# Kernel tuning notes

Measured on AMD Instinct MI355X. Metric: run time of the kernel, lower is better.

## Reference

```python
import jax, jax.numpy as jnp
import numpy as np

B, L, H, NH, DH, FF, NL, REL = 2, 1024, 256, 8, 32, 1024, 2, 100
SCALE = np.sqrt(DH).astype(np.float32)
EPS = 1e-5


def _ln(x, g, b):
    m = jnp.mean(x, axis=-1, keepdims=True)
    v = jnp.mean(jnp.square(x - m), axis=-1, keepdims=True)
    return (x - m) * jax.lax.rsqrt(v + EPS) * g + b


def setup_inputs() -> dict:
    key = jax.random.key(0)
    ks = jax.random.split(key, 20)
    s = 0.02
    Ek = jax.random.normal(ks[0], (REL, DH), jnp.float32) * s
    Ev = jax.random.normal(ks[1], (REL, DH), jnp.float32) * s
    Ek = Ek.at[0].set(0.0)  # padding_idx=0
    Ev = Ev.at[0].set(0.0)
    return {
        "inputs": jax.random.normal(ks[2], (B, L, H), jnp.float32),
        "Wq": jax.random.normal(ks[3], (NL, H, H), jnp.float32) * s,
        "Wk": jax.random.normal(ks[4], (NL, H, H), jnp.float32) * s,
        "Wv": jax.random.normal(ks[5], (NL, H, H), jnp.float32) * s,
        "Wo": jax.random.normal(ks[6], (NL, H, H), jnp.float32) * s,
        "bo": jnp.zeros((NL, H), jnp.float32),
        "W1": jax.random.normal(ks[7], (NL, H, FF), jnp.float32) * s,
        "b1": jnp.zeros((NL, FF), jnp.float32),
        "W2": jax.random.normal(ks[8], (NL, FF, H), jnp.float32) * s,
        "b2": jnp.zeros((NL, H), jnp.float32),
        "ln1_g": jnp.ones((NL, H), jnp.float32),
        "ln1_b": jnp.zeros((NL, H), jnp.float32),
        "ln2_g": jnp.ones((NL, H), jnp.float32),
        "ln2_b": jnp.zeros((NL, H), jnp.float32),
        "Ek": Ek,
        "Ev": Ev,
        "relations": jax.random.randint(ks[9], (B, L, L), 0, REL, jnp.int32),
        "relations_mask": jax.random.randint(ks[10], (B, L, L), 0, 2, jnp.int32).astype(bool),
    }


def reference(inputs, Wq, Wk, Wv, Wo, bo, W1, b1, W2, b2,
              ln1_g, ln1_b, ln2_g, ln2_b, Ek, Ev, relations, relations_mask):
    # relation embeddings shared across layers and heads: (B,L,L,DH)
    rel_k = Ek[relations]
    rel_v = Ev[relations]
    neg = relations_mask.astype(jnp.float32) * (-1e20)  # (B,L,L)
    x = inputs
    for l in range(NL):
        q = (x @ Wq[l]).reshape(B, L, NH, DH)
        k = (x @ Wk[l]).reshape(B, L, NH, DH)
        v = (x @ Wv[l]).reshape(B, L, NH, DH)
        # scores: q.(k_j + rel_k[i,j]) decomposed to avoid (B,H,L,L,DH)
        e = (jnp.einsum('bihd,bjhd->bhij', q, k)
             + jnp.einsum('bihd,bijd->bhij', q, rel_k)) / SCALE
        e = e + neg[:, None, :, :]
        a = jax.nn.softmax(e, axis=-1)  # (B,NH,L,L)
        o = (jnp.einsum('bhij,bjhd->bihd', a, v)
             + jnp.einsum('bhij,bijd->bihd', a, rel_v)).reshape(B, L, H)
        o = o @ Wo[l] + bo[l]
        x = _ln(x + o, ln1_g[l], ln1_b[l])
        ff = jax.nn.relu(x @ W1[l] + b1[l]) @ W2[l] + b2[l]
        x = _ln(x + ff, ln2_g[l], ln2_b[l])
    return x
```

## Files before the change

### kernel.cpp

```cpp
#include <hip/hip_runtime.h>


typedef unsigned short ushortt;
typedef __attribute__((ext_vector_type(8))) short short8;
typedef __attribute__((ext_vector_type(4))) float f32x4;

__device__ __forceinline__ ushortt f2bf(float f) {
  union { float f; unsigned int u; } c; c.f = f;
  unsigned int r = c.u + 0x7fffu + ((c.u >> 16) & 1u);
  return (ushortt)(r >> 16);
}
__device__ __forceinline__ unsigned int pk2(float a, float b) {
  return (unsigned int)f2bf(a) | ((unsigned int)f2bf(b) << 16);
}

__global__ void wcvt_all_k(const float* __restrict__ Wq, const float* __restrict__ Wk,
                           const float* __restrict__ Wv, const float* __restrict__ Wo,
                           const float* __restrict__ W1, const float* __restrict__ W2,
                           ushortt* __restrict__ wbuf) {
  int i = blockIdx.x * blockDim.x + threadIdx.x;
  int st = gridDim.x * blockDim.x;
  for (; i < 1572864; i += st) {
    int l = (i >= 786432) ? 1 : 0;
    int e = i - (l ? 786432 : 0);
    size_t o_w = (size_t)l * 65536, o_w1 = (size_t)l * 262144;
    float v;
    if (e < 262144) {
      int which = e >> 16;
      int loc = e & 65535;
      int k = loc & 255, n = loc >> 8;
      const float* W = (which == 0) ? Wq : (which == 1) ? Wk : (which == 2) ? Wv : Wo;
      v = W[o_w + ((size_t)k << 8) + n];
    } else if (e < 524288) {
      int loc = e - 262144;
      int k = loc & 255, n = loc >> 8;
      v = W1[o_w1 + ((size_t)k << 10) + n];
    } else {
      int loc = e - 524288;
      int k = loc & 1023, n = loc >> 10;
      v = W2[o_w1 + ((size_t)k << 8) + n];
    }
    wbuf[i] = f2bf(v);
  }
}

__global__ __launch_bounds__(256) void cvt_bf_k(
    const float* __restrict__ in, ushortt* __restrict__ out, int n) {
  int idx = (blockIdx.x * 256 + threadIdx.x) * 8;
  if (idx >= n) return;
  float4 f0 = *(const float4*)(in + idx);
  float4 f1 = *(const float4*)(in + idx + 4);
  uint4 u;
  u.x = pk2(f0.x, f0.y); u.y = pk2(f0.z, f0.w);
  u.z = pk2(f1.x, f1.y); u.w = pk2(f1.z, f1.w);
  *(uint4*)(out + idx) = u;
}

__global__ __launch_bounds__(256) void relpack_k(
    const int* __restrict__ rel, const int* __restrict__ msk,
    unsigned char* __restrict__ relc2,
    const float* __restrict__ Ev, float* __restrict__ EvT) {
  int g = blockIdx.x * blockDim.x + threadIdx.x;
  const int4* r4 = (const int4*)rel;
  const int4* m4 = (const int4*)msk;
  int4 r = r4[g];
  int4 m = m4[g];
  int b = g >> 18;
  int rem = g & 262143;
  int i = rem >> 8;
  int j4 = (rem & 255) << 2;
  size_t base = ((size_t)b << 20) + ((size_t)(i >> 3) << 13) + (i & 7);
  relc2[base + ((size_t)(j4 + 0) << 3)] = (unsigned char)(m.x ? 128 : r.x);
  relc2[base + ((size_t)(j4 + 1) << 3)] = (unsigned char)(m.y ? 128 : r.y);
  relc2[base + ((size_t)(j4 + 2) << 3)] = (unsigned char)(m.z ? 128 : r.z);
  relc2[base + ((size_t)(j4 + 3) << 3)] = (unsigned char)(m.w ? 128 : r.w);
  if (g < 3200) {
    int d = g / 100, rr = g - d * 100;
    EvT[d * 100 + rr] = Ev[(rr << 5) + d];
  }
}

__device__ __forceinline__ void mgemm_body(
    const ushortt* __restrict__ A, const ushortt* __restrict__ BT,
    const float* __restrict__ bias, size_t boff,
    float* __restrict__ C, ushortt* __restrict__ cbf,
    int m0, int n0, int N, int K, int kbeg, int kend, int relu, int kvmode)
{
  __shared__ ushortt As[64 * 72];
  __shared__ ushortt Bs[64 * 72];
  int tid = threadIdx.x;
  int wv = tid >> 6, lane = tid & 63;
  int quad = lane >> 4, mr = lane & 15;
  int sm = tid >> 2, k16 = (tid & 3) << 4;

  const ushortt* ap = A + (size_t)(m0 + sm) * K + k16;
  const ushortt* bp = BT + (size_t)(n0 + sm) * K + k16;

  uint4 ra0 = *(const uint4*)(ap + kbeg);
  uint4 ra1 = *(const uint4*)(ap + kbeg + 8);
  uint4 rb0 = *(const uint4*)(bp + kbeg);
  uint4 rb1 = *(const uint4*)(bp + kbeg + 8);

  f32x4 acc[4] = {};
  for (int k0 = kbeg; k0 < kend; k0 += 64) {
    *(uint4*)(&As[sm * 72 + k16])     = ra0;
    *(uint4*)(&As[sm * 72 + k16 + 8]) = ra1;
    *(uint4*)(&Bs[sm * 72 + k16])     = rb0;
    *(uint4*)(&Bs[sm * 72 + k16 + 8]) = rb1;
    __syncthreads();
    if (k0 + 64 < kend) {
      ra0 = *(const uint4*)(ap + k0 + 64);
      ra1 = *(const uint4*)(ap + k0 + 72);
      rb0 = *(const uint4*)(bp + k0 + 64);
      rb1 = *(const uint4*)(bp + k0 + 72);
    }
#pragma unroll
    for (int kh = 0; kh < 2; ++kh) {
      short8 af = *(const short8*)(&As[(wv * 16 + mr) * 72 + (kh << 5) + quad * 8]);
#pragma unroll
      for (int nt = 0; nt < 4; ++nt) {
        short8 bf = *(const short8*)(&Bs[(nt * 16 + mr) * 72 + (kh << 5) + quad * 8]);
        acc[nt] = __builtin_amdgcn_mfma_f32_16x16x32_bf16(af, bf, acc[nt], 0, 0, 0);
      }
    }
    __syncthreads();
  }
#pragma unroll
  for (int nt = 0; nt < 4; ++nt) {
#pragma unroll
    for (int r = 0; r < 4; ++r) {
      int m = m0 + wv * 16 + quad * 4 + r;
      int n = n0 + nt * 16 + mr;
      float v = acc[nt][r];
      if (bias) v += bias[boff + n];
      if (relu) v = fmaxf(v, 0.f);
      if (kvmode == 1) {
        int b = m >> 10, i = m & 1023, h = n >> 5, d = n & 31;
        cbf[(size_t)(((b << 3) + h) * 32 + d) * 1024 + i] = f2bf(v);
      } else if (kvmode == 2) {
        int b = m >> 10, i = m & 1023, h = n >> 5, d = n & 31;
        cbf[(size_t)(((b << 3) + h) * 1024 + i) * 32 + d] = f2bf(v);
      } else if (cbf) {
        cbf[(size_t)m * N + n] = f2bf(v);
      } else {
        C[(size_t)m * N + n] = v;
      }
    }
  }
}

__global__ __launch_bounds__(256) void mgemm_k(
    const ushortt* __restrict__ A, const ushortt* __restrict__ BT,
    const float* __restrict__ bias, size_t boff,
    float* __restrict__ C0, float* __restrict__ C1, ushortt* __restrict__ cbf,
    int N, int K, int relu)
{
  int kidx = blockIdx.z;
  int kc = K / gridDim.z;
  int kbeg = kidx * kc;
  mgemm_body(A, BT, kidx ? nullptr : bias, boff,
             kidx ? C1 : C0, cbf,
             blockIdx.y * 64, blockIdx.x * 64, N, K, kbeg, kbeg + kc, relu, 0);
}

__global__ __launch_bounds__(256) void mqkv_k(
    const ushortt* __restrict__ xbf, const ushortt* __restrict__ WT,
    float* __restrict__ q, ushortt* __restrict__ kbf, ushortt* __restrict__ vTbf)
{
  int sel = blockIdx.x >> 2;
  const ushortt* BT = WT + (size_t)sel * 65536;
  int mode = (sel == 1) ? 2 : (sel == 2) ? 1 : 0;
  mgemm_body(xbf, BT, nullptr, 0,
             (sel == 0) ? q : nullptr,
             (sel == 1) ? kbf : (sel == 2) ? vTbf : nullptr,
             blockIdx.y * 64, (blockIdx.x & 3) * 64, 256, 256, 0, 256, 0, mode);
}

__global__ __launch_bounds__(256) void attn_mf8_k(
    const float* __restrict__ q, const ushortt* __restrict__ kbf,
    const ushortt* __restrict__ vTbf, const float* __restrict__ Ek,
    const float* __restrict__ EvT, const unsigned char* __restrict__ relc2,
    ushortt* __restrict__ out)
{
  __shared__ ushortt pbf[8 * 1028];
  __shared__ float regA[1072];
  __shared__ float wbin[8 * 108];

  int tid = threadIdx.x;
  int wv = tid >> 6, lane = tid & 63;
  int quad = lane >> 4, mr = lane & 15;
  int tile = blockIdx.x & 127;
  int h = (blockIdx.x >> 7) & 7;
  int b = blockIdx.x >> 10;
  int i0 = tile << 3;

  int iqsel = quad & 1;
  int iq = iqsel << 2;
  int jofs = ((quad >> 1) << 4) + mr;
  int jbase = wv << 8;
  const unsigned int* rc2 =
      (const unsigned int*)(relc2 + (((size_t)(b << 7) + tile) << 13));
  unsigned int rcw[8];
#pragma unroll
  for (int t = 0; t < 8; ++t)
    rcw[t] = rc2[(((jbase + (t << 5) + jofs)) << 1) + iqsel];

  float* qs = regA;
  float* expq = regA + 264;

  {
    int i = tid >> 5, d = tid & 31;
    qs[i * 33 + d] = q[(((size_t)(b * 1024 + i0 + i) * 8 + h) << 5) + d]
                     * 0.17677669529663687f;
  }
  for (int p = tid; p < 864; p += 256) wbin[p] = 0.f;
  __syncthreads();

  for (int p = tid; p < 800; p += 256) {
    int i = p / 100, r = p - i * 100;
    const float* ep = Ek + (r << 5);
    float s = 0.f;
#pragma unroll
    for (int d = 0; d < 32; ++d) s += qs[i * 33 + d] * ep[d];
    expq[i * 101 + r] = __expf(s);
  }
  __syncthreads();

  short8 qf;
#pragma unroll
  for (int jj = 0; jj < 8; ++jj)
    ((ushortt*)&qf)[jj] = f2bf(qs[(mr & 7) * 33 + quad * 8 + jj]);

  const ushortt* ks = kbf + ((size_t)(b * 8 + h) << 15);
  const ushortt* vs = vTbf + ((size_t)(b * 8 + h) << 15);

  short8 kfa = *(const short8*)(ks + ((size_t)(jbase + mr) << 5) + quad * 8);
  short8 kfb = *(const short8*)(ks + ((size_t)(jbase + 16 + mr) << 5) + quad * 8);
#pragma unroll
  for (int t = 0; t < 8; ++t) {
    int j0 = jbase + (t << 5);
    short8 ka = kfa, kb = kfb;
    if (t < 7) {
      kfa = *(const short8*)(ks + ((size_t)(j0 + 32 + mr) << 5) + quad * 8);
      kfb = *(const short8*)(ks + ((size_t)(j0 + 48 + mr) << 5) + quad * 8);
    }
    f32x4 z = {};
    f32x4 sa = __builtin_amdgcn_mfma_f32_16x16x32_bf16(qf, ka, z, 0, 0, 0);
    f32x4 sb = __builtin_amdgcn_mfma_f32_16x16x32_bf16(qf, kb, z, 0, 0, 0);
    int j = j0 + jofs;
    unsigned int w = rcw[t];
#pragma unroll
    for (int r = 0; r < 4; ++r) {
      int i = iq + r;
      float sv = (quad >= 2) ? sb[r] : sa[r];
      unsigned int c = (w >> (r << 3)) & 255u;
      float p = 0.f;
      if (c < 128u) {
        p = __expf(sv) * expq[i * 101 + (int)c];
        atomicAdd(&wbin[i * 108 + (int)c], p);
      }
      pbf[i * 1028 + j] = f2bf(p);
    }
  }
  __syncthreads();

  float* pvpart = regA;
  float* pvtot  = regA + 256;
  int d0 = (wv & 1) << 4;
  int k0 = (wv >> 1) << 9;
  int prow = (mr & 7) * 1028;
  f32x4 acc0 = {}, acc1 = {};
  short8 vf = *(const short8*)(vs + ((size_t)(d0 + mr) << 10) + k0 + quad * 8);
#pragma unroll
  for (int kt = 0; kt < 16; ++kt) {
    int kk = k0 + (kt << 5);
    short8 vcur = vf;
    if (kt < 15)
      vf = *(const short8*)(vs + ((size_t)(d0 + mr) << 10) + k0 + ((kt + 1) << 5) + quad * 8);
    short8 pf = *(const short8*)(&pbf[prow + kk + quad * 8]);
    if (kt & 1)
      acc1 = __builtin_amdgcn_mfma_f32_16x16x32_bf16(pf, vcur, acc1, 0, 0, 0);
    else
      acc0 = __builtin_amdgcn_mfma_f32_16x16x32_bf16(pf, vcur, acc0, 0, 0, 0);
  }
  f32x4 acc;
#pragma unroll
  for (int r = 0; r < 4; ++r) acc[r] = acc0[r] + acc1[r];
  if (wv >= 2 && quad < 2) {
#pragma unroll
    for (int r = 0; r < 4; ++r)
      pvpart[((wv & 1) << 7) + (quad * 4 + r) * 16 + mr] = acc[r];
  }
  __syncthreads();
  if (wv < 2 && quad < 2) {
#pragma unroll
    for (int r = 0; r < 4; ++r) {
      int i = quad * 4 + r;
      pvtot[i * 32 + d0 + mr] = acc[r] + pvpart[((wv & 1) << 7) + i * 16 + mr];
    }
  }
  __syncthreads();

  {
    int i = tid >> 5, d = tid & 31;
    const float4* evt = (const float4*)(EvT + d * 100);
    const float4* wb4 = (const float4*)(&wbin[i * 108]);
    float e0 = 0.f, e1 = 0.f, e2 = 0.f, e3 = 0.f;
    float s0 = 0.f, s1 = 0.f, s2 = 0.f, s3 = 0.f;
#pragma unroll
    for (int rq = 0; rq < 25; ++rq) {
      float4 e4 = evt[rq];
      float4 w4 = wb4[rq];
      e0 += w4.x * e4.x; s0 += w4.x;
      e1 += w4.y * e4.y; s1 += w4.y;
      e2 += w4.z * e4.z; s2 += w4.z;
      e3 += w4.w * e4.w; s3 += w4.w;
    }
    float ev = (e0 + e1) + (e2 + e3);
    float den = (s0 + s1) + (s2 + s3);
    out[(((size_t)(b * 1024 + i0 + i) * 8 + h) << 5) + d] =
        f2bf((pvtot[i * 32 + d] + ev) / den);
  }
}

__global__ __launch_bounds__(256) void ln_k(
    const float* __restrict__ x, const float* __restrict__ o,
    const float* __restrict__ o2,
    const float* __restrict__ g, const float* __restrict__ bta, size_t eoff,
    float* __restrict__ xo, ushortt* __restrict__ xbf, float* __restrict__ fout)
{
  __shared__ float red[256];
  int row = blockIdx.x, t = threadIdx.x;
  size_t idx = (size_t)row * 256 + t;
  float r = x[idx] + o[idx];
  if (o2) r += o2[idx];
  red[t] = r;
  __syncthreads();
  for (int off = 128; off > 0; off >>= 1) {
    if (t < off) red[t] += red[t + off];
    __syncthreads();
  }
  float mean = red[0] * (1.f / 256.f);
  __syncthreads();
  float dv = r - mean;
  red[t] = dv * dv;
  __syncthreads();
  for (int off = 128; off > 0; off >>= 1) {
    if (t < off) red[t] += red[t + off];
    __syncthreads();
  }
  float var = red[0] * (1.f / 256.f);
  float val = dv * rsqrtf(var + 1e-5f) * g[eoff + t] + bta[eoff + t];
  xo[idx] = val;
  xbf[idx] = f2bf(val);
  if (fout) fout[idx] = val;
}

extern "C" void kernel_launch(void* const* d_in, const int* in_sizes, int n_in,
                              void* d_out, int out_size, void* d_ws, size_t ws_size,
                              hipStream_t stream) {
  const float* inp  = (const float*)d_in[0];
  const float* Wq   = (const float*)d_in[1];
  const float* Wk   = (const float*)d_in[2];
  const float* Wv   = (const float*)d_in[3];
  const float* Wo   = (const float*)d_in[4];
  const float* bo   = (const float*)d_in[5];
  const float* W1   = (const float*)d_in[6];
  const float* b1   = (const float*)d_in[7];
  const float* W2   = (const float*)d_in[8];
  const float* b2   = (const float*)d_in[9];
  const float* ln1g = (const float*)d_in[10];
  const float* ln1b = (const float*)d_in[11];
  const float* ln2g = (const float*)d_in[12];
  const float* ln2b = (const float*)d_in[13];
  const float* Ek   = (const float*)d_in[14];
  const float* Ev   = (const float*)d_in[15];
  const int*   rel  = (const int*)d_in[16];
  const int*   msk  = (const int*)d_in[17];

  const size_t SZ = 524288;
  float* x        = (float*)d_ws;
  float* q        = x + SZ;
  ushortt* kbf    = (ushortt*)(q + SZ);
  ushortt* vTbf   = kbf + SZ;
  ushortt* attnbf = vTbf + SZ;
  ushortt* xbf    = attnbf + SZ;
  float* tmp      = (float*)(xbf + SZ);
  ushortt* wbuf   = (ushortt*)(tmp + SZ);
  unsigned char* relc2 = (unsigned char*)(wbuf + 1572864);
  float* EvT      = (float*)(relc2 + 2097152);
  float* tmp2     = (float*)((char*)EvT + 16384);
  ushortt* inpbf  = (ushortt*)tmp2;
  ushortt* ffh    = (ushortt*)q;

  dim3 blk(256);
  wcvt_all_k<<<3072, blk, 0, stream>>>(Wq, Wk, Wv, Wo, W1, W2, wbuf);
  relpack_k<<<2048, blk, 0, stream>>>(rel, msk, relc2, Ev, EvT);
  cvt_bf_k<<<256, blk, 0, stream>>>(inp, inpbf, 524288);

  for (int l = 0; l < 2; ++l) {
    size_t o_b  = (size_t)l * 256;
    size_t o_b1 = (size_t)l * 1024;
    const ushortt* xinbf = (l == 0) ? inpbf : xbf;
    const float* xin = (l == 0) ? inp : x;
    ushortt* wl = wbuf + (size_t)l * 786432;

    mqkv_k<<<dim3(12, 32), blk, 0, stream>>>(xinbf, wl, q, kbf, vTbf);

    attn_mf8_k<<<2048, blk, 0, stream>>>(q, kbf, vTbf, Ek, EvT, relc2, attnbf);

    mgemm_k<<<dim3(4, 32, 2), blk, 0, stream>>>(attnbf, wl + 196608,
                                                bo, o_b, tmp, tmp2, nullptr,
                                                256, 256, 0);
    ln_k<<<2048, blk, 0, stream>>>(xin, tmp, tmp2, ln1g, ln1b, o_b, x, xbf, nullptr);

    mgemm_k<<<dim3(16, 32, 1), blk, 0, stream>>>(xbf, wl + 262144,
                                                 b1, o_b1, nullptr, nullptr, ffh,
                                                 1024, 256, 1);
    mgemm_k<<<dim3(4, 32, 2), blk, 0, stream>>>(ffh, wl + 524288,
                                                b2, o_b, tmp, tmp2, nullptr,
                                                256, 1024, 0);
    ln_k<<<2048, blk, 0, stream>>>(x, tmp, tmp2, ln2g, ln2b, o_b, x, xbf,
                                   (l == 1) ? (float*)d_out : nullptr);
  }
}
```

Before: 387.5 us.

## Split q·Ek exponent table into separate kernel and emit pre-scaled bf16 q

Moves the per-tile exp(q·Ek) relation-score table out of the attention kernel into a new eqk_k kernel that stages Ek in shared memory and writes the table to global memory. The QKV GEMM now also writes a pre-scaled bf16 copy of q in head-major layout, so attention loads its MFMA fragment directly instead of converting from fp32 shared memory. This removes one barrier and the serial dot-product prologue from the attention kernel, aiming to shorten its critical path and shrink its shared memory. The cost is an extra launch and a global round trip of about 6.5 MB for the table per layer.

Measured after the change: 372.1 us. -4.0%, faster.

```diff
diff --git a/kernel.cpp b/kernel.cpp
--- a/kernel.cpp
+++ b/kernel.cpp
@@ -80,6 +80,37 @@
   }
 }
 
+__global__ __launch_bounds__(256) void eqk_k(
+    const float* __restrict__ q, const float* __restrict__ Ek,
+    float* __restrict__ eqk) {
+  __shared__ float qs[8 * 33];
+  __shared__ float ek[100 * 33];
+  int tid = threadIdx.x;
+  int bid = blockIdx.x;
+  int tile = bid & 127;
+  int h = (bid >> 7) & 7;
+  int b = bid >> 10;
+  int i0 = tile << 3;
+  {
+    int i = tid >> 5, d = tid & 31;
+    qs[i * 33 + d] = q[(((size_t)(b * 1024 + i0 + i) * 8 + h) << 5) + d]
+                     * 0.17677669529663687f;
+  }
+  for (int p = tid; p < 3200; p += 256) {
+    int r = p >> 5, d = p & 31;
+    ek[r * 33 + d] = Ek[p];
+  }
+  __syncthreads();
+  float* eo = eqk + (size_t)bid * 800;
+  for (int p = tid; p < 800; p += 256) {
+    int i = p / 100, r = p - i * 100;
+    float s = 0.f;
+#pragma unroll
+    for (int d = 0; d < 32; ++d) s += qs[i * 33 + d] * ek[r * 33 + d];
+    eo[p] = __expf(s);
+  }
+}
+
 __device__ __forceinline__ void mgemm_body(
     const ushortt* __restrict__ A, const ushortt* __restrict__ BT,
     const float* __restrict__ bias, size_t boff,
@@ -134,7 +165,12 @@
       float v = acc[nt][r];
       if (bias) v += bias[boff + n];
       if (relu) v = fmaxf(v, 0.f);
-      if (kvmode == 1) {
+      if (kvmode == 3) {
+        C[(size_t)m * N + n] = v;
+        int b = m >> 10, i = m & 1023, h = n >> 5, d = n & 31;
+        cbf[(size_t)(((b << 3) + h) * 1024 + i) * 32 + d] =
+            f2bf(v * 0.17677669529663687f);
+      } else if (kvmode == 1) {
         int b = m >> 10, i = m & 1023, h = n >> 5, d = n & 31;
         cbf[(size_t)(((b << 3) + h) * 32 + d) * 1024 + i] = f2bf(v);
       } else if (kvmode == 2) {
@@ -165,33 +201,35 @@
 
 __global__ __launch_bounds__(256) void mqkv_k(
     const ushortt* __restrict__ xbf, const ushortt* __restrict__ WT,
-    float* __restrict__ q, ushortt* __restrict__ kbf, ushortt* __restrict__ vTbf)
+    float* __restrict__ q, ushortt* __restrict__ qbf,
+    ushortt* __restrict__ kbf, ushortt* __restrict__ vTbf)
 {
   int sel = blockIdx.x >> 2;
   const ushortt* BT = WT + (size_t)sel * 65536;
-  int mode = (sel == 1) ? 2 : (sel == 2) ? 1 : 0;
+  int mode = (sel == 0) ? 3 : (sel == 1) ? 2 : 1;
   mgemm_body(xbf, BT, nullptr, 0,
              (sel == 0) ? q : nullptr,
-             (sel == 1) ? kbf : (sel == 2) ? vTbf : nullptr,
+             (sel == 0) ? qbf : (sel == 1) ? kbf : vTbf,
              blockIdx.y * 64, (blockIdx.x & 3) * 64, 256, 256, 0, 256, 0, mode);
 }
 
 __global__ __launch_bounds__(256) void attn_mf8_k(
-    const float* __restrict__ q, const ushortt* __restrict__ kbf,
-    const ushortt* __restrict__ vTbf, const float* __restrict__ Ek,
+    const ushortt* __restrict__ qbf, const ushortt* __restrict__ kbf,
+    const ushortt* __restrict__ vTbf, const float* __restrict__ eqk,
     const float* __restrict__ EvT, const unsigned char* __restrict__ relc2,
     ushortt* __restrict__ out)
 {
   __shared__ ushortt pbf[8 * 1028];
-  __shared__ float regA[1072];
+  __shared__ float expq[800];
   __shared__ float wbin[8 * 108];
 
   int tid = threadIdx.x;
   int wv = tid >> 6, lane = tid & 63;
   int quad = lane >> 4, mr = lane & 15;
-  int tile = blockIdx.x & 127;
-  int h = (blockIdx.x >> 7) & 7;
-  int b = blockIdx.x >> 10;
+  int bid = blockIdx.x;
+  int tile = bid & 127;
+  int h = (bid >> 7) & 7;
+  int b = bid >> 10;
   int i0 = tile << 3;
 
   int iqsel = quad & 1;
@@ -205,37 +243,19 @@
   for (int t = 0; t < 8; ++t)
     rcw[t] = rc2[(((jbase + (t << 5) + jofs)) << 1) + iqsel];
 
-  float* qs = regA;
-  float* expq = regA + 264;
-
-  {
-    int i = tid >> 5, d = tid & 31;
-    qs[i * 33 + d] = q[(((size_t)(b * 1024 + i0 + i) * 8 + h) << 5) + d]
-                     * 0.17677669529663687f;
-  }
+  const float* eo = eqk + (size_t)bid * 800;
+  for (int p = tid; p < 800; p += 256) expq[p] = eo[p];
   for (int p = tid; p < 864; p += 256) wbin[p] = 0.f;
-  __syncthreads();
-
-  for (int p = tid; p < 800; p += 256) {
-    int i = p / 100, r = p - i * 100;
-    const float* ep = Ek + (r << 5);
-    float s = 0.f;
-#pragma unroll
-    for (int d = 0; d < 32; ++d) s += qs[i * 33 + d] * ep[d];
-    expq[i * 101 + r] = __expf(s);
-  }
-  __syncthreads();
-
-  short8 qf;
-#pragma unroll
-  for (int jj = 0; jj < 8; ++jj)
-    ((ushortt*)&qf)[jj] = f2bf(qs[(mr & 7) * 33 + quad * 8 + jj]);
+
+  const ushortt* qsrc = qbf + ((size_t)(b * 8 + h) << 15);
+  short8 qf = *(const short8*)(qsrc + (((size_t)i0 + (mr & 7)) << 5) + quad * 8);
 
   const ushortt* ks = kbf + ((size_t)(b * 8 + h) << 15);
   const ushortt* vs = vTbf + ((size_t)(b * 8 + h) << 15);
-
   short8 kfa = *(const short8*)(ks + ((size_t)(jbase + mr) << 5) + quad * 8);
   short8 kfb = *(const short8*)(ks + ((size_t)(jbase + 16 + mr) << 5) + quad * 8);
+  __syncthreads();
+
 #pragma unroll
   for (int t = 0; t < 8; ++t) {
     int j0 = jbase + (t << 5);
@@ -256,7 +276,7 @@
       unsigned int c = (w >> (r << 3)) & 255u;
       float p = 0.f;
       if (c < 128u) {
-        p = __expf(sv) * expq[i * 101 + (int)c];
+        p = __expf(sv) * expq[i * 100 + (int)c];
         atomicAdd(&wbin[i * 108 + (int)c], p);
       }
       pbf[i * 1028 + j] = f2bf(p);
@@ -264,8 +284,8 @@
   }
   __syncthreads();
 
-  float* pvpart = regA;
-  float* pvtot  = regA + 256;
+  float* pvpart = expq;
+  float* pvtot  = expq + 256;
   int d0 = (wv & 1) << 4;
   int k0 = (wv >> 1) << 9;
   int prow = (mr & 7) * 1028;
@@ -391,6 +411,8 @@
   float* EvT      = (float*)(relc2 + 2097152);
   float* tmp2     = (float*)((char*)EvT + 16384);
   ushortt* inpbf  = (ushortt*)tmp2;
+  ushortt* qbf    = (ushortt*)(tmp2 + SZ);
+  float* eqkbuf   = (float*)(qbf + SZ);
   ushortt* ffh    = (ushortt*)q;
 
   dim3 blk(256);
@@ -405,9 +427,11 @@
     const float* xin = (l == 0) ? inp : x;
     ushortt* wl = wbuf + (size_t)l * 786432;
 
-    mqkv_k<<<dim3(12, 32), blk, 0, stream>>>(xinbf, wl, q, kbf, vTbf);
-
-    attn_mf8_k<<<2048, blk, 0, stream>>>(q, kbf, vTbf, Ek, EvT, relc2, attnbf);
+    mqkv_k<<<dim3(12, 32), blk, 0, stream>>>(xinbf, wl, q, qbf, kbf, vTbf);
+
+    eqk_k<<<2048, blk, 0, stream>>>(q, Ek, eqkbuf);
+
+    attn_mf8_k<<<2048, blk, 0, stream>>>(qbf, kbf, vTbf, eqkbuf, EvT, relc2, attnbf);
 
     mgemm_k<<<dim3(4, 32, 2), blk, 0, stream>>>(attnbf, wl + 196608,
                                                 bo, o_b, tmp, tmp2, nullptr,
```
